# Optimization experiments

Measured on AMD Instinct MI355X. Metric: run time of the kernel, lower is better.

The kernel has to match this reference:

```python
import jax, jax.numpy as jnp
import numpy as np

WIDTH, BITS, RANGE_SCALE = 16, 8, 32
EPS_MAX = RANGE_SCALE * BITS / 2 ** BITS  # = 1.0 for these hw constants


def _rshift(v, s):
    # v >> s with mathematically-correct result for s >= bitwidth (torch/hw: -> 0)
    return jnp.where(s >= 32, 0, jnp.right_shift(v, jnp.minimum(s, 31)))


def _ita_softmax(x):
    B, H, S, K = x.shape
    groups = K // WIDTH
    x3 = x.reshape(B * H, S, K).astype(jnp.int32)
    # (groups, BH, S, WIDTH) so we can scan the streaming loop over groups
    chunks = x3.reshape(B * H, S, groups, WIDTH).transpose(2, 0, 1, 3)

    def step(carry, chunk):
        eps_sum, gmax = carry  # (BH,S) int32 each
        cmax = chunk.max(axis=-1)
        mask = cmax > gmax
        max_shift = jnp.floor((cmax - gmax).astype(jnp.float32) * EPS_MAX + 0.5).astype(jnp.int32)
        shift_sum = jnp.where(mask, max_shift, 0)
        gmax = jnp.where(mask, cmax, gmax)
        diff = gmax[..., None] - chunk  # (BH,S,WIDTH), >= 0
        shift = jnp.floor(diff.astype(jnp.float32) * EPS_MAX + 0.5).astype(jnp.int32)
        exp_sum = _rshift(2 ** BITS, shift).sum(axis=-1).astype(jnp.int32)
        eps_sum = _rshift(eps_sum, shift_sum) + exp_sum
        return (eps_sum, gmax), None

    init = (jnp.zeros((B * H, S), jnp.int32), jnp.full((B * H, S), -128, jnp.int32))
    (eps_sum, gmax), _ = jax.lax.scan(step, init, chunks)

    # floor(((2^bits - 1) * 2^bits) / sum) ; eps_sum >= 2^bits always (max elem -> shift 0)
    inv = jnp.floor_divide(jnp.int32((2 ** BITS - 1) * 2 ** BITS), eps_sum)
    diff = gmax[..., None] - x3
    shift = jnp.floor(diff.astype(jnp.float32) * EPS_MAX + 0.5).astype(jnp.int32)
    res = _rshift(inv[..., None], shift).astype(jnp.uint8)  # floor(inv / 2^shift)
    return res.reshape(B, H, S, K)


def setup_inputs() -> dict:
    key = jax.random.key(0)
    x = jax.random.randint(key, (2, 16, 2048, 2048), -128, 128, dtype=jnp.int32)
    return {"x": x}


def reference(x):
    return _ita_softmax(x)
```

## Files before the change

kernel.cpp:

```cpp
#include <hip/hip_runtime.h>


constexpr int K = 2048;
constexpr int SEG_STRIDE = 36;
constexpr int ROW_LDS = SEG_STRIDE * (K / 32);
constexpr int WAVES_PER_BLOCK = 4;

__global__ __launch_bounds__(256) void ita_softmax_kernel(
    const int* __restrict__ x, int* __restrict__ out, int nrows) {
  __shared__ int lds[WAVES_PER_BLOCK][ROW_LDS];
  const int lane = threadIdx.x & 63;
  const int wave = threadIdx.x >> 6;
  const int row = blockIdx.x * WAVES_PER_BLOCK + wave;
  const bool active = (row < nrows);
  int* myLds = lds[wave];

  if (active) {
    const int* xr = x + (size_t)row * K;
#pragma unroll
    for (int j = 0; j < 8; ++j) {
      int4 v = *reinterpret_cast<const int4*>(xr + 256 * j + 4 * lane);
      int addr = 288 * j + SEG_STRIDE * (lane >> 3) + 4 * (lane & 7);
      *reinterpret_cast<int4*>(myLds + addr) = v;
    }
  }
  __syncthreads();

  if (active) {
    int xa[32];
#pragma unroll
    for (int k = 0; k < 8; ++k) {
      int4 v = *reinterpret_cast<const int4*>(myLds + SEG_STRIDE * lane + 4 * k);
      xa[4 * k + 0] = v.x; xa[4 * k + 1] = v.y;
      xa[4 * k + 2] = v.z; xa[4 * k + 3] = v.w;
    }
    int cmax0 = xa[0], cmax1 = xa[16];
#pragma unroll
    for (int i = 1; i < 16; ++i) {
      cmax0 = max(cmax0, xa[i]);
      cmax1 = max(cmax1, xa[16 + i]);
    }
    int inc = max(cmax0, cmax1);
#pragma unroll
    for (int d = 1; d < 64; d <<= 1) {
      int t = __shfl_up(inc, d);
      if (lane >= d) inc = max(inc, t);
    }
    int E = __shfl_up(inc, 1);
    if (lane == 0) E = -128;
    const int P0 = max(E, cmax0);
    const int P1 = max(P0, cmax1);
    const int M = __shfl(inc, 63);

    int s0 = 0, s1 = 0;
#pragma unroll
    for (int i = 0; i < 16; ++i) {
      s0 += 256 >> min(P0 - xa[i], 31);
      s1 += 256 >> min(P1 - xa[16 + i], 31);
    }
    const int pk0 = (int)(((unsigned)(P0 - E) << 16) | (unsigned)s0);
    const int pk1 = (int)(((unsigned)(P1 - P0) << 16) | (unsigned)s1);

    int eps = 0;
    for (int src = 0; src < 64; ++src) {
      unsigned a = (unsigned)__shfl(pk0, src);
      unsigned b = (unsigned)__shfl(pk1, src);
      eps = (eps >> min((int)(a >> 16), 31)) + (int)(a & 0xffffu);
      eps = (eps >> min((int)(b >> 16), 31)) + (int)(b & 0xffffu);
    }
    const int inv = 65280 / eps;

    int* orow = out + (size_t)row * K;
#pragma unroll
    for (int j = 0; j < 8; ++j) {
      int addr = 288 * j + SEG_STRIDE * (lane >> 3) + 4 * (lane & 7);
      int4 v = *reinterpret_cast<const int4*>(myLds + addr);
      int4 o;
      o.x = inv >> min(M - v.x, 31);
      o.y = inv >> min(M - v.y, 31);
      o.z = inv >> min(M - v.z, 31);
      o.w = inv >> min(M - v.w, 31);
      *reinterpret_cast<int4*>(orow + 256 * j + 4 * lane) = o;
    }
  }
}

extern "C" void kernel_launch(void* const* d_in, const int* in_sizes, int n_in,
                              void* d_out, int out_size, void* d_ws, size_t ws_size,
                              hipStream_t stream) {
  const int* x = (const int*)d_in[0];
  int* out = (int*)d_out;
  const int nrows = in_sizes[0] / K;
  const int blocks = (nrows + WAVES_PER_BLOCK - 1) / WAVES_PER_BLOCK;
  ita_softmax_kernel<<<blocks, 256, 0, stream>>>(x, out, nrows);
}
```

Before: 204.7 us.

## Replace LDS transpose with register-resident row and quad-shuffle group reductions

Removes the shared-memory staging and transpose of each row. Each lane now keeps its coalesced int4 loads in registers, and the 16-element groups are formed by 4-lane quads using xor shuffles. Per-chunk prefix maxima are computed with shuffles. The serial eps recurrence now uses readlane over 128 scalar steps instead of 128 vector shuffles. This drops LDS traffic and the __syncthreads, but adds a prefix-scan per chunk (8 scans instead of 1).

Measured after the change: 207.2 us. About the same (+1.2%).

```diff
diff --git a/kernel.cpp b/kernel.cpp
--- a/kernel.cpp
+++ b/kernel.cpp
@@ -2,86 +2,68 @@
 
 
 constexpr int K = 2048;
-constexpr int SEG_STRIDE = 36;
-constexpr int ROW_LDS = SEG_STRIDE * (K / 32);
 constexpr int WAVES_PER_BLOCK = 4;
 
 __global__ __launch_bounds__(256) void ita_softmax_kernel(
     const int* __restrict__ x, int* __restrict__ out, int nrows) {
-  __shared__ int lds[WAVES_PER_BLOCK][ROW_LDS];
   const int lane = threadIdx.x & 63;
   const int wave = threadIdx.x >> 6;
   const int row = blockIdx.x * WAVES_PER_BLOCK + wave;
-  const bool active = (row < nrows);
-  int* myLds = lds[wave];
+  if (row >= nrows) return;
 
-  if (active) {
-    const int* xr = x + (size_t)row * K;
+  const int* xr = x + (size_t)row * K;
+  int4 xv[8];
+  int pk[8];
+  int A = -128;
+
 #pragma unroll
-    for (int j = 0; j < 8; ++j) {
-      int4 v = *reinterpret_cast<const int4*>(xr + 256 * j + 4 * lane);
-      int addr = 288 * j + SEG_STRIDE * (lane >> 3) + 4 * (lane & 7);
-      *reinterpret_cast<int4*>(myLds + addr) = v;
+  for (int j = 0; j < 8; ++j) {
+    xv[j] = *reinterpret_cast<const int4*>(xr + 256 * j + 4 * lane);
+    const int4 v = xv[j];
+    int gm = max(max(v.x, v.y), max(v.z, v.w));
+    gm = max(gm, __shfl_xor(gm, 1));
+    gm = max(gm, __shfl_xor(gm, 2));
+    int cp = gm;
+#pragma unroll
+    for (int d = 4; d < 64; d <<= 1) {
+      int t = __shfl_up(cp, d);
+      if (lane >= d) cp = max(cp, t);
+    }
+    int ecp = __shfl_up(cp, 4);
+    if (lane < 4) ecp = (int)0x80000000;
+    const int P = max(A, cp);
+    const int Pp = max(A, ecp);
+    const int dd = min(P - Pp, 31);
+    int sp = (256 >> min(P - v.x, 31)) + (256 >> min(P - v.y, 31)) +
+             (256 >> min(P - v.z, 31)) + (256 >> min(P - v.w, 31));
+    sp += __shfl_xor(sp, 1);
+    sp += __shfl_xor(sp, 2);
+    pk[j] = (dd << 16) | sp;
+    A = max(A, __shfl(cp, 63));
+  }
+  const int M = A;
+
+  int eps = 0;
+#pragma unroll
+  for (int j = 0; j < 8; ++j) {
+#pragma unroll
+    for (int a = 0; a < 16; ++a) {
+      const unsigned u = (unsigned)__builtin_amdgcn_readlane(pk[j], 4 * a);
+      eps = (eps >> (u >> 16)) + (int)(u & 0xffffu);
     }
   }
-  __syncthreads();
+  const int inv = 65280 / eps;
 
-  if (active) {
-    int xa[32];
+  int* orow = out + (size_t)row * K;
 #pragma unroll
-    for (int k = 0; k < 8; ++k) {
-      int4 v = *reinterpret_cast<const int4*>(myLds + SEG_STRIDE * lane + 4 * k);
-      xa[4 * k + 0] = v.x; xa[4 * k + 1] = v.y;
-      xa[4 * k + 2] = v.z; xa[4 * k + 3] = v.w;
-    }
-    int cmax0 = xa[0], cmax1 = xa[16];
-#pragma unroll
-    for (int i = 1; i < 16; ++i) {
-      cmax0 = max(cmax0, xa[i]);
-      cmax1 = max(cmax1, xa[16 + i]);
-    }
-    int inc = max(cmax0, cmax1);
-#pragma unroll
-    for (int d = 1; d < 64; d <<= 1) {
-      int t = __shfl_up(inc, d);
-      if (lane >= d) inc = max(inc, t);
-    }
-    int E = __shfl_up(inc, 1);
-    if (lane == 0) E = -128;
-    const int P0 = max(E, cmax0);
-    const int P1 = max(P0, cmax1);
-    const int M = __shfl(inc, 63);
-
-    int s0 = 0, s1 = 0;
-#pragma unroll
-    for (int i = 0; i < 16; ++i) {
-      s0 += 256 >> min(P0 - xa[i], 31);
-      s1 += 256 >> min(P1 - xa[16 + i], 31);
-    }
-    const int pk0 = (int)(((unsigned)(P0 - E) << 16) | (unsigned)s0);
-    const int pk1 = (int)(((unsigned)(P1 - P0) << 16) | (unsigned)s1);
-
-    int eps = 0;
-    for (int src = 0; src < 64; ++src) {
-      unsigned a = (unsigned)__shfl(pk0, src);
-      unsigned b = (unsigned)__shfl(pk1, src);
-      eps = (eps >> min((int)(a >> 16), 31)) + (int)(a & 0xffffu);
-      eps = (eps >> min((int)(b >> 16), 31)) + (int)(b & 0xffffu);
-    }
-    const int inv = 65280 / eps;
-
-    int* orow = out + (size_t)row * K;
-#pragma unroll
-    for (int j = 0; j < 8; ++j) {
-      int addr = 288 * j + SEG_STRIDE * (lane >> 3) + 4 * (lane & 7);
-      int4 v = *reinterpret_cast<const int4*>(myLds + addr);
-      int4 o;
-      o.x = inv >> min(M - v.x, 31);
-      o.y = inv >> min(M - v.y, 31);
-      o.z = inv >> min(M - v.z, 31);
-      o.w = inv >> min(M - v.w, 31);
-      *reinterpret_cast<int4*>(orow + 256 * j + 4 * lane) = o;
-    }
+  for (int j = 0; j < 8; ++j) {
+    const int4 v = xv[j];
+    int4 o;
+    o.x = inv >> min(M - v.x, 31);
+    o.y = inv >> min(M - v.y, 31);
+    o.z = inv >> min(M - v.z, 31);
+    o.w = inv >> min(M - v.w, 31);
+    *reinterpret_cast<int4*>(orow + 256 * j + 4 * lane) = o;
   }
 }
 
```
